# Optimization experiments

Measured on AMD Instinct MI355X. Metric: run time of the kernel, lower is better.

Reference implementation:

```python
import jax, jax.numpy as jnp
import numpy as np

DIM, HEADS, WS, SHIFT = 192, 6, 8, 4
EPS = 1e-5


def layer_norm(x, g, b):
    mu = jnp.mean(x, axis=-1, keepdims=True)
    var = jnp.mean(jnp.square(x - mu), axis=-1, keepdims=True)
    return (x - mu) * jax.lax.rsqrt(var + EPS) * g + b


def window_partition(x, ws):
    # x: [B, H, W, C] -> [B*nW, ws*ws, C]
    B, H, W, C = x.shape
    x = x.reshape(B, H // ws, ws, W // ws, ws, C)
    return x.transpose(0, 1, 3, 2, 4, 5).reshape(-1, ws * ws, C)


def window_merge(win, ws, B, H, W, C):
    x = win.reshape(B, H // ws, W // ws, ws, ws, C)
    return x.transpose(0, 1, 3, 2, 4, 5).reshape(B, H, W, C)


def make_shift_mask(H, W, ws, shift):
    # standard Swin attention mask for shifted windows (host-side constant)
    img = np.zeros((H, W), dtype=np.float32)
    cnt = 0
    slices = (slice(0, -ws), slice(-ws, -shift), slice(-shift, None))
    for hs in slices:
        for wsl in slices:
            img[hs, wsl] = cnt
            cnt += 1
    m = img.reshape(H // ws, ws, W // ws, ws).transpose(0, 2, 1, 3).reshape(-1, ws * ws)  # [nW, N]
    diff = m[:, None, :] - m[:, :, None]
    return jnp.asarray(np.where(diff != 0, -100.0, 0.0).astype(np.float32))  # [nW, N, N]


def swin_attention(x, qkv_w, qkv_b, proj_w, proj_b, shift):
    B, H, W, C = x.shape
    h, d = HEADS, C // HEADS
    scale = 1.0 / jnp.sqrt(jnp.asarray(d, x.dtype))
    if shift > 0:
        x = jnp.roll(x, shift=(-shift, -shift), axis=(1, 2))
    win = window_partition(x, WS)                       # [Bn, N, C]
    Bn, N, _ = win.shape
    qkv = win @ qkv_w + qkv_b                           # [Bn, N, 3C]
    qkv = qkv.reshape(Bn, N, 3, h, d).transpose(2, 0, 3, 1, 4)
    q, k, v = qkv[0], qkv[1], qkv[2]                    # [Bn, h, N, d]
    attn = jnp.einsum('bhnd,bhmd->bhnm', q, k) * scale  # [Bn, h, N, N]
    if shift > 0:
        mask = make_shift_mask(H, W, WS, shift)         # [nW, N, N]
        nW = mask.shape[0]
        attn = attn.reshape(Bn // nW, nW, h, N, N) + mask[None, :, None]
        attn = attn.reshape(Bn, h, N, N)
    attn = jax.nn.softmax(attn, axis=-1)
    out = jnp.einsum('bhnm,bhmd->bhnd', attn, v)        # [Bn, h, N, d]
    out = out.transpose(0, 2, 1, 3).reshape(Bn, N, C)
    out = out @ proj_w + proj_b
    out = window_merge(out, WS, B, H, W, C)
    if shift > 0:
        out = jnp.roll(out, shift=(shift, shift), axis=(1, 2))
    return out


def setup_inputs() -> dict:
    key = jax.random.key(0)
    ks = jax.random.split(key, 6)
    B, H, W, C = 8, 128, 128, DIM
    s = 0.02
    return {
        'x': jax.random.normal(ks[0], (B, H, W, C), jnp.float32),
        'ln1_g': jnp.ones((C,), jnp.float32),
        'ln1_b': jnp.zeros((C,), jnp.float32),
        'qkv1_w': jax.random.normal(ks[1], (C, 3 * C), jnp.float32) * s,
        'qkv1_b': jnp.zeros((3 * C,), jnp.float32),
        'proj1_w': jax.random.normal(ks[2], (C, C), jnp.float32) * s,
        'proj1_b': jnp.zeros((C,), jnp.float32),
        'ln2_g': jnp.ones((C,), jnp.float32),
        'ln2_b': jnp.zeros((C,), jnp.float32),
        'qkv2_w': jax.random.normal(ks[3], (C, 3 * C), jnp.float32) * s,
        'qkv2_b': jnp.zeros((3 * C,), jnp.float32),
        'proj2_w': jax.random.normal(ks[4], (C, C), jnp.float32) * s,
        'proj2_b': jnp.zeros((C,), jnp.float32),
    }


def reference(x, ln1_g, ln1_b, qkv1_w, qkv1_b, proj1_w, proj1_b,
              ln2_g, ln2_b, qkv2_w, qkv2_b, proj2_w, proj2_b):
    # W-MSA branch (mlp1 is an empty Sequential -> identity)
    y = layer_norm(x, ln1_g, ln1_b)
    x = x + swin_attention(y, qkv1_w, qkv1_b, proj1_w, proj1_b, shift=0)
    # SW-MSA branch (mlp2 is identity)
    y = layer_norm(x, ln2_g, ln2_b)
    x = x + swin_attention(y, qkv2_w, qkv2_b, proj2_w, proj2_b, shift=SHIFT)
    return x
```

## Files before the change

kernel.cpp:

```cpp
#include <hip/hip_runtime.h>

typedef unsigned int   u32;
typedef unsigned short u16;
typedef __bf16 bf16x8 __attribute__((ext_vector_type(8)));
typedef float  f32x4  __attribute__((ext_vector_type(4)));

__device__ __forceinline__ u16 f2bf(float f) {
    u32 u = __builtin_bit_cast(u32, f);
    u += 0x7FFFu + ((u >> 16) & 1u);
    return (u16)(u >> 16);
}
__device__ __forceinline__ u32 pk2bf(float a, float b) {
    return (u32)f2bf(a) | ((u32)f2bf(b) << 16);
}
__device__ __forceinline__ bf16x8 ldfrag(const u16* p) {
    return __builtin_bit_cast(bf16x8, *reinterpret_cast<const uint4*>(p));
}

__device__ __forceinline__ u32 swz(u32 i) { return i ^ ((i >> 3) & 7u); }

template<int SHIFT>
__global__ __launch_bounds__(768) void swin_branch(
    const float* __restrict__ xin, float* __restrict__ xout,
    const float* __restrict__ ln_g, const float* __restrict__ ln_b,
    const u16*   __restrict__ wqkv_t,
    const float* __restrict__ qkv_b,
    const u16*   __restrict__ wproj_t,
    const float* __restrict__ proj_b)
{
    __shared__ __align__(16) u16 smem[49152];
    __shared__ float red1[2][6][64];
    __shared__ float red2[2][6][64];
    constexpr u32 QOFF = 12288;

    const int tid  = threadIdx.x;
    const int win  = (tid >= 384) ? 1 : 0;
    const int lt   = tid - win*384;
    const int wid  = lt >> 6;
    const int lane = lt & 63;
    const int lr   = lane & 15;
    const int lg   = lane >> 4;
    const u32 lsw  = swz((u32)lane);
    const u32 SB   = (u32)win * 24576u;

    const int Wid = blockIdx.x*2 + win;
    const int b   = Wid >> 8;
    const int wy  = (Wid >> 4) & 15;
    const int wx  = Wid & 15;

    {
        const int ty = lane >> 3, tx = lane & 7;
        const int shy = (wy*8 + ty + SHIFT) & 127;
        const int shx = (wx*8 + tx + SHIFT) & 127;
        const float* xp = xin + ((size_t)((b*128 + shy)*128 + shx))*192 + wid*32;
        float xv[32];
        float s1 = 0.f, s2 = 0.f;
        #pragma unroll
        for (int j = 0; j < 8; ++j) {
            float4 v = reinterpret_cast<const float4*>(xp)[j];
            xv[j*4+0]=v.x; xv[j*4+1]=v.y; xv[j*4+2]=v.z; xv[j*4+3]=v.w;
            s1 += v.x+v.y+v.z+v.w;
            s2 += v.x*v.x + v.y*v.y + v.z*v.z + v.w*v.w;
        }
        red1[win][wid][lane] = s1; red2[win][wid][lane] = s2;
        __syncthreads();
        float a1 = 0.f, a2 = 0.f;
        #pragma unroll
        for (int w = 0; w < 6; ++w) { a1 += red1[win][w][lane]; a2 += red2[win][w][lane]; }
        const float mu = a1 * (1.f/192.f);
        const float rs = rsqrtf(a2 * (1.f/192.f) - mu*mu + 1e-5f);
        const float* gp = ln_g + wid*32;
        const float* bp = ln_b + wid*32;
        const u32 yblk = SB + (u32)((lg*6 + wid)*512);
        #pragma unroll
        for (int cc8 = 0; cc8 < 4; ++cc8) {
            u32 pk[4];
            #pragma unroll
            for (int q = 0; q < 4; ++q) {
                int j = cc8*8 + q*2;
                float y0 = (xv[j]   - mu)*rs*gp[j]   + bp[j];
                float y1 = (xv[j+1] - mu)*rs*gp[j+1] + bp[j+1];
                pk[q] = pk2bf(y0, y1);
            }
            *reinterpret_cast<uint4*>(&smem[yblk + swz((u32)(lr + 16*cc8))*8]) =
                make_uint4(pk[0],pk[1],pk[2],pk[3]);
        }
    }
    __syncthreads();

    uint2 kpk[4][2];
    uint2 vpk[4][2];
    {
        {
            f32x4 acc[4][4];
            #pragma unroll
            for (int mi=0; mi<4; ++mi)
                #pragma unroll
                for (int t=0; t<4; ++t) acc[mi][t] = f32x4{0.f,0.f,0.f,0.f};
            #pragma unroll
            for (int ks=0; ks<6; ++ks) {
                bf16x8 af[4];
                #pragma unroll
                for (int mi=0; mi<4; ++mi)
                    af[mi] = ldfrag(&smem[SB + (u32)((mi*6+ks)*512) + lsw*8]);
                bf16x8 bw[4];
                #pragma unroll
                for (int t=0; t<4; ++t)
                    bw[t] = ldfrag(&wqkv_t[((t>>1)*192 + wid*32 + (t&1)*16 + lr)*192 + 32*ks + 8*lg]);
                #pragma unroll
                for (int mi=0; mi<4; ++mi)
                    #pragma unroll
                    for (int t=0; t<4; ++t)
                        acc[mi][t] = __builtin_amdgcn_mfma_f32_16x16x32_bf16(af[mi], bw[t], acc[mi][t], 0,0,0);
            }
            #pragma unroll
            for (int t=0; t<2; ++t) {
                const float bias = qkv_b[wid*32 + t*16 + lr];
                const u32 lphi   = (u32)(16*(2*t + (lr>>3)));
                #pragma unroll
                for (int mi=0; mi<4; ++mi)
                    #pragma unroll
                    for (int rg=0; rg<4; ++rg) {
                        const u32 pos = (u32)(4*lg + rg) + lphi;
                        smem[SB + QOFF + (u32)(wid*2048) + mi*512 + swz(pos)*8 + (lr&7)] =
                            f2bf((acc[mi][t][rg] + bias) * 0.1767766952966369f);
                    }
            }
            #pragma unroll
            for (int t2=0; t2<2; ++t2) {
                const float bias = qkv_b[192 + wid*32 + t2*16 + lr];
                #pragma unroll
                for (int mi=0; mi<4; ++mi)
                    kpk[mi][t2] = make_uint2(
                        pk2bf(acc[mi][2+t2][0] + bias, acc[mi][2+t2][1] + bias),
                        pk2bf(acc[mi][2+t2][2] + bias, acc[mi][2+t2][3] + bias));
            }
        }
        {
            f32x4 acc[4][2];
            #pragma unroll
            for (int mi=0; mi<4; ++mi)
                #pragma unroll
                for (int t=0; t<2; ++t) acc[mi][t] = f32x4{0.f,0.f,0.f,0.f};
            #pragma unroll
            for (int ks=0; ks<6; ++ks) {
                bf16x8 af[4];
                #pragma unroll
                for (int mi=0; mi<4; ++mi)
                    af[mi] = ldfrag(&smem[SB + (u32)((mi*6+ks)*512) + lsw*8]);
                bf16x8 bw[2];
                #pragma unroll
                for (int t=0; t<2; ++t)
                    bw[t] = ldfrag(&wqkv_t[(384 + wid*32 + t*16 + lr)*192 + 32*ks + 8*lg]);
                #pragma unroll
                for (int mi=0; mi<4; ++mi)
                    #pragma unroll
                    for (int t=0; t<2; ++t)
                        acc[mi][t] = __builtin_amdgcn_mfma_f32_16x16x32_bf16(af[mi], bw[t], acc[mi][t], 0,0,0);
            }
            #pragma unroll
            for (int tv=0; tv<2; ++tv) {
                const float bias = qkv_b[384 + wid*32 + tv*16 + lr];
                #pragma unroll
                for (int mi=0; mi<4; ++mi)
                    vpk[mi][tv] = make_uint2(
                        pk2bf(acc[mi][tv][0] + bias, acc[mi][tv][1] + bias),
                        pk2bf(acc[mi][tv][2] + bias, acc[mi][tv][3] + bias));
            }
        }
    }
    __syncthreads();

    float rsum[4][4];
    f32x4 o_[4][2];
    {
        const u32 W  = SB + (u32)(wid*512);
        const u32 qb = SB + QOFF + (u32)(wid*2048);
        #define BLK(s) ((u32)(s)*3072u + W)

        #pragma unroll
        for (int t2=0; t2<2; ++t2) {
            const u32 lphi = (u32)(16*(2*t2 + (lr>>3)));
            #pragma unroll
            for (int mi=0; mi<4; ++mi) {
                const u32 a0 = BLK(mi) + (lr&7);
                smem[a0 + swz((u32)(4*lg+0) + lphi)*8] = (u16)(kpk[mi][t2].x);
                smem[a0 + swz((u32)(4*lg+1) + lphi)*8] = (u16)(kpk[mi][t2].x >> 16);
                smem[a0 + swz((u32)(4*lg+2) + lphi)*8] = (u16)(kpk[mi][t2].y);
                smem[a0 + swz((u32)(4*lg+3) + lphi)*8] = (u16)(kpk[mi][t2].y >> 16);
            }
        }
        bf16x8 aq[4], bk[4];
        #pragma unroll
        for (int mi=0; mi<4; ++mi) aq[mi] = ldfrag(&smem[qb + mi*512 + lsw*8]);
        #pragma unroll
        for (int ni=0; ni<4; ++ni) bk[ni] = ldfrag(&smem[BLK(ni) + lsw*8]);
        __builtin_amdgcn_sched_barrier(0);

        #pragma unroll
        for (int tv=0; tv<2; ++tv)
            #pragma unroll
            for (int mi=0; mi<4; ++mi) {
                const u32 pos = (u32)(lr + 16*(2*(mi&1) + (lg>>1)));
                *reinterpret_cast<uint2*>(
                    &smem[BLK(tv*2 + (mi>>1)) + swz(pos)*8 + 4*(lg&1)]) = vpk[mi][tv];
            }

        int kl[4];
        if constexpr (SHIFT > 0) {
            #pragma unroll
            for (int ni=0; ni<4; ++ni) {
                const int col = 16*ni + lr;
                const int hu = wy*8 + (col>>3);
                const int wu = wx*8 + (col&7);
                kl[ni] = ((hu >= 124) ? 2 : (hu >= 120 ? 1 : 0))*3
                       + ((wu >= 124) ? 2 : (wu >= 120 ? 1 : 0));
            }
        }
        u32 p16[4][4][2];
        #pragma unroll
        for (int mi=0; mi<4; ++mi) {
            f32x4 sr[4];
            #pragma unroll
            for (int ni=0; ni<4; ++ni)
                sr[ni] = __builtin_amdgcn_mfma_f32_16x16x32_bf16(aq[mi], bk[ni],
                             f32x4{0.f,0.f,0.f,0.f}, 0,0,0);
            #pragma unroll
            for (int rg=0; rg<4; ++rg) {
                int rl = 0;
                if constexpr (SHIFT > 0) {
                    const int row = 16*mi + 4*lg + rg;
                    const int hu = wy*8 + (row>>3);
                    const int wu = wx*8 + (row&7);
                    rl = ((hu >= 124) ? 2 : (hu >= 120 ? 1 : 0))*3
                       + ((wu >= 124) ? 2 : (wu >= 120 ? 1 : 0));
                }
                #pragma unroll
                for (int ni=0; ni<4; ++ni) {
                    float e = __expf(sr[ni][rg]);
                    if constexpr (SHIFT > 0)
                        e = (rl == kl[ni]) ? e : 0.f;
                    sr[ni][rg] = e;
                }
            }
            #pragma unroll
            for (int ni=0; ni<4; ++ni) {
                p16[mi][ni][0] = pk2bf(sr[ni][0], sr[ni][1]);
                p16[mi][ni][1] = pk2bf(sr[ni][2], sr[ni][3]);
            }
        }

        bf16x8 ap0[4], ap1[4];
        #pragma unroll
        for (int mi=0; mi<4; ++mi)
            #pragma unroll
            for (int ni=0; ni<2; ++ni)
                #pragma unroll
                for (int rg=0; rg<4; ++rg) {
                    const u32 pos = (u32)(4*lg + rg + 16*(2*ni + (lr>>3)));
                    smem[qb + mi*512 + swz(pos)*8 + (lr&7)] =
                        (u16)(p16[mi][ni][rg>>1] >> (16*(rg&1)));
                }
        #pragma unroll
        for (int mi=0; mi<4; ++mi) ap0[mi] = ldfrag(&smem[qb + mi*512 + lsw*8]);
        __builtin_amdgcn_sched_barrier(0);
        #pragma unroll
        for (int mi=0; mi<4; ++mi)
            #pragma unroll
            for (int ni=2; ni<4; ++ni)
                #pragma unroll
                for (int rg=0; rg<4; ++rg) {
                    const u32 pos = (u32)(4*lg + rg + 16*(2*(ni-2) + (lr>>3)));
                    smem[qb + mi*512 + swz(pos)*8 + (lr&7)] =
                        (u16)(p16[mi][ni][rg>>1] >> (16*(rg&1)));
                }
        #pragma unroll
        for (int mi=0; mi<4; ++mi) ap1[mi] = ldfrag(&smem[qb + mi*512 + lsw*8]);
        __builtin_amdgcn_sched_barrier(0);

        bf16x8 vones;
        #pragma unroll
        for (int j=0; j<8; ++j) vones[j] = (__bf16)1.0f;
        #pragma unroll
        for (int mi=0; mi<4; ++mi) {
            f32x4 racc = __builtin_amdgcn_mfma_f32_16x16x32_bf16(ap0[mi], vones,
                             f32x4{0.f,0.f,0.f,0.f}, 0,0,0);
            racc = __builtin_amdgcn_mfma_f32_16x16x32_bf16(ap1[mi], vones, racc, 0,0,0);
            #pragma unroll
            for (int rg=0; rg<4; ++rg)
                rsum[mi][rg] = __builtin_amdgcn_rcpf(racc[rg]);
        }

        bf16x8 bv[2][2];
        #pragma unroll
        for (int tv=0; tv<2; ++tv)
            #pragma unroll
            for (int ksv=0; ksv<2; ++ksv)
                bv[tv][ksv] = ldfrag(&smem[BLK(tv*2+ksv) + lsw*8]);

        #pragma unroll
        for (int mi=0; mi<4; ++mi)
            #pragma unroll
            for (int tv=0; tv<2; ++tv) {
                o_[mi][tv] = __builtin_amdgcn_mfma_f32_16x16x32_bf16(ap0[mi], bv[tv][0],
                                 f32x4{0.f,0.f,0.f,0.f}, 0,0,0);
                o_[mi][tv] = __builtin_amdgcn_mfma_f32_16x16x32_bf16(ap1[mi], bv[tv][1],
                                 o_[mi][tv], 0,0,0);
            }
        __builtin_amdgcn_sched_barrier(0);

        #pragma unroll
        for (int mi=0; mi<4; ++mi)
            #pragma unroll
            for (int tv=0; tv<2; ++tv)
                #pragma unroll
                for (int rg=0; rg<4; ++rg) {
                    const u32 pos = (u32)(4*lg + rg + 16*(2*tv + (lr>>3)));
                    smem[BLK(mi) + swz(pos)*8 + (lr&7)] = f2bf(o_[mi][tv][rg] * rsum[mi][rg]);
                }
        #undef BLK
    }
    __syncthreads();

    {
        f32x4 a2[4][2];
        #pragma unroll
        for (int mi=0; mi<4; ++mi)
            #pragma unroll
            for (int ni=0; ni<2; ++ni) a2[mi][ni] = f32x4{0.f,0.f,0.f,0.f};
        #pragma unroll
        for (int ks=0; ks<6; ++ks) {
            bf16x8 af[4], bw[2];
            #pragma unroll
            for (int mi=0; mi<4; ++mi)
                af[mi] = ldfrag(&smem[SB + (u32)((mi*6+ks)*512) + lsw*8]);
            #pragma unroll
            for (int ni=0; ni<2; ++ni)
                bw[ni] = ldfrag(&wproj_t[(wid*32 + 16*ni + lr)*192 + 32*ks + 8*lg]);
            #pragma unroll
            for (int mi=0; mi<4; ++mi)
                #pragma unroll
                for (int ni=0; ni<2; ++ni)
                    a2[mi][ni] = __builtin_amdgcn_mfma_f32_16x16x32_bf16(af[mi], bw[ni], a2[mi][ni], 0,0,0);
        }
        #pragma unroll
        for (int ni=0; ni<2; ++ni) {
            const int c  = wid*32 + 16*ni + lr;
            const float pb = proj_b[c];
            #pragma unroll
            for (int mi=0; mi<4; ++mi)
                #pragma unroll
                for (int rg=0; rg<4; ++rg) {
                    const int row = 16*mi + 4*lg + rg;
                    const int ty = row >> 3, tx = row & 7;
                    const int shy = (wy*8 + ty + SHIFT) & 127;
                    const int shx = (wx*8 + tx + SHIFT) & 127;
                    const size_t idx = ((size_t)((b*128 + shy)*128 + shx))*192 + c;
                    xout[idx] = xin[idx] + a2[mi][ni][rg] + pb;
                }
        }
    }
}

__global__ void prep_weights(const float* __restrict__ qkv1, const float* __restrict__ proj1,
                             const float* __restrict__ qkv2, const float* __restrict__ proj2,
                             u16* __restrict__ ws)
{
    const int i = blockIdx.x*blockDim.x + threadIdx.x;
    if (i < 110592) {
        const int n = i / 192, k = i - n*192;
        ws[i]          = f2bf(qkv1[k*576 + n]);
        ws[147456 + i] = f2bf(qkv2[k*576 + n]);
    }
    if (i < 36864) {
        const int n = i / 192, k = i - n*192;
        ws[110592 + i] = f2bf(proj1[k*192 + n]);
        ws[258048 + i] = f2bf(proj2[k*192 + n]);
    }
}

extern "C" void kernel_launch(void* const* d_in, const int* in_sizes, int n_in,
                              void* d_out, int out_size, void* d_ws, size_t ws_size,
                              hipStream_t stream)
{
    const float* x       = (const float*)d_in[0];
    const float* ln1_g   = (const float*)d_in[1];
    const float* ln1_b   = (const float*)d_in[2];
    const float* qkv1_w  = (const float*)d_in[3];
    const float* qkv1_b  = (const float*)d_in[4];
    const float* proj1_w = (const float*)d_in[5];
    const float* proj1_b = (const float*)d_in[6];
    const float* ln2_g   = (const float*)d_in[7];
    const float* ln2_b   = (const float*)d_in[8];
    const float* qkv2_w  = (const float*)d_in[9];
    const float* qkv2_b  = (const float*)d_in[10];
    const float* proj2_w = (const float*)d_in[11];
    const float* proj2_b = (const float*)d_in[12];
    float* out = (float*)d_out;
    u16*   wsp = (u16*)d_ws;

    prep_weights<<<dim3(432), dim3(256), 0, stream>>>(qkv1_w, proj1_w, qkv2_w, proj2_w, wsp);
    swin_branch<0><<<dim3(1024), dim3(768), 0, stream>>>(x,   out, ln1_g, ln1_b,
                                                         wsp,        qkv1_b, wsp+110592, proj1_b);
    swin_branch<4><<<dim3(1024), dim3(768), 0, stream>>>(out, out, ln2_g, ln2_b,
                                                         wsp+147456, qkv2_b, wsp+258048, proj2_b);
}
```

Baseline: 268.0 us.

## Transpose attention MFMA operands for packed LDS stores and hardware bf16 conversion

Swaps MFMA operand order so the QKV, score and PV accumulators come out transposed. Each lane can then write four contiguous bf16 values with one 64-bit LDS store instead of four scalar 16-bit stores. The software bf16 rounding is replaced by the v_cvt_pk_bf16_f32 instruction, and log2(e) is folded into the Q scale so exp2f can replace __expf. Row sums are now computed with a ones-matrix as the A operand, and V is staged in the Q buffer. This reworks the fragment layout across all attention stages, which risks subtle indexing or mask-orientation errors.

```diff
diff --git a/kernel.cpp b/kernel.cpp
--- a/kernel.cpp
+++ b/kernel.cpp
@@ -10,8 +10,10 @@
     u += 0x7FFFu + ((u >> 16) & 1u);
     return (u16)(u >> 16);
 }
-__device__ __forceinline__ u32 pk2bf(float a, float b) {
-    return (u32)f2bf(a) | ((u32)f2bf(b) << 16);
+__device__ __forceinline__ u32 cvtpk(float a, float b) {
+    u32 r;
+    asm("v_cvt_pk_bf16_f32 %0, %1, %2" : "=v"(r) : "v"(a), "v"(b));
+    return r;
 }
 __device__ __forceinline__ bf16x8 ldfrag(const u16* p) {
     return __builtin_bit_cast(bf16x8, *reinterpret_cast<const uint4*>(p));
@@ -32,6 +34,7 @@
     __shared__ float red1[2][6][64];
     __shared__ float red2[2][6][64];
     constexpr u32 QOFF = 12288;
+    constexpr float QSC = 0.17677669529663689f * 1.4426950408889634f;
 
     const int tid  = threadIdx.x;
     const int win  = (tid >= 384) ? 1 : 0;
@@ -80,7 +83,7 @@
                 int j = cc8*8 + q*2;
                 float y0 = (xv[j]   - mu)*rs*gp[j]   + bp[j];
                 float y1 = (xv[j+1] - mu)*rs*gp[j+1] + bp[j+1];
-                pk[q] = pk2bf(y0, y1);
+                pk[q] = cvtpk(y0, y1);
             }
             *reinterpret_cast<uint4*>(&smem[yblk + swz((u32)(lr + 16*cc8))*8]) =
                 make_uint4(pk[0],pk[1],pk[2],pk[3]);
@@ -111,29 +114,31 @@
                 for (int mi=0; mi<4; ++mi)
                     #pragma unroll
                     for (int t=0; t<4; ++t)
-                        acc[mi][t] = __builtin_amdgcn_mfma_f32_16x16x32_bf16(af[mi], bw[t], acc[mi][t], 0,0,0);
+                        acc[mi][t] = __builtin_amdgcn_mfma_f32_16x16x32_bf16(bw[t], af[mi], acc[mi][t], 0,0,0);
             }
             #pragma unroll
             for (int t=0; t<2; ++t) {
-                const float bias = qkv_b[wid*32 + t*16 + lr];
-                const u32 lphi   = (u32)(16*(2*t + (lr>>3)));
-                #pragma unroll
-                for (int mi=0; mi<4; ++mi)
-                    #pragma unroll
-                    for (int rg=0; rg<4; ++rg) {
-                        const u32 pos = (u32)(4*lg + rg) + lphi;
-                        smem[SB + QOFF + (u32)(wid*2048) + mi*512 + swz(pos)*8 + (lr&7)] =
-                            f2bf((acc[mi][t][rg] + bias) * 0.1767766952966369f);
-                    }
+                const float4 b4 = *reinterpret_cast<const float4*>(&qkv_b[wid*32 + t*16 + 4*lg]);
+                const u32 chunk = (u32)lr + 16u*(u32)(2*t + (lg>>1));
+                #pragma unroll
+                for (int mi=0; mi<4; ++mi) {
+                    float v0 = (acc[mi][t][0] + b4.x) * QSC;
+                    float v1 = (acc[mi][t][1] + b4.y) * QSC;
+                    float v2 = (acc[mi][t][2] + b4.z) * QSC;
+                    float v3 = (acc[mi][t][3] + b4.w) * QSC;
+                    *reinterpret_cast<uint2*>(
+                        &smem[SB + QOFF + (u32)(wid*2048) + mi*512 + swz(chunk)*8 + 4*(lg&1)]) =
+                        make_uint2(cvtpk(v0,v1), cvtpk(v2,v3));
+                }
             }
             #pragma unroll
             for (int t2=0; t2<2; ++t2) {
-                const float bias = qkv_b[192 + wid*32 + t2*16 + lr];
+                const float4 b4 = *reinterpret_cast<const float4*>(&qkv_b[192 + wid*32 + t2*16 + 4*lg]);
                 #pragma unroll
                 for (int mi=0; mi<4; ++mi)
                     kpk[mi][t2] = make_uint2(
-                        pk2bf(acc[mi][2+t2][0] + bias, acc[mi][2+t2][1] + bias),
-                        pk2bf(acc[mi][2+t2][2] + bias, acc[mi][2+t2][3] + bias));
+                        cvtpk(acc[mi][2+t2][0] + b4.x, acc[mi][2+t2][1] + b4.y),
+                        cvtpk(acc[mi][2+t2][2] + b4.z, acc[mi][2+t2][3] + b4.w));
             }
         }
         {
@@ -164,160 +169,147 @@
                 #pragma unroll
                 for (int mi=0; mi<4; ++mi)
                     vpk[mi][tv] = make_uint2(
-                        pk2bf(acc[mi][tv][0] + bias, acc[mi][tv][1] + bias),
-                        pk2bf(acc[mi][tv][2] + bias, acc[mi][tv][3] + bias));
+                        cvtpk(acc[mi][tv][0] + bias, acc[mi][tv][1] + bias),
+                        cvtpk(acc[mi][tv][2] + bias, acc[mi][tv][3] + bias));
             }
         }
     }
     __syncthreads();
 
-    float rsum[4][4];
-    f32x4 o_[4][2];
+    float rsum[4];
+    f32x4 o_[2][4];
     {
         const u32 W  = SB + (u32)(wid*512);
-        const u32 qb = SB + QOFF + (u32)(wid*2048);
+        const u32 QB = SB + QOFF + (u32)(wid*2048);
         #define BLK(s) ((u32)(s)*3072u + W)
 
         #pragma unroll
         for (int t2=0; t2<2; ++t2) {
-            const u32 lphi = (u32)(16*(2*t2 + (lr>>3)));
-            #pragma unroll
-            for (int mi=0; mi<4; ++mi) {
-                const u32 a0 = BLK(mi) + (lr&7);
-                smem[a0 + swz((u32)(4*lg+0) + lphi)*8] = (u16)(kpk[mi][t2].x);
-                smem[a0 + swz((u32)(4*lg+1) + lphi)*8] = (u16)(kpk[mi][t2].x >> 16);
-                smem[a0 + swz((u32)(4*lg+2) + lphi)*8] = (u16)(kpk[mi][t2].y);
-                smem[a0 + swz((u32)(4*lg+3) + lphi)*8] = (u16)(kpk[mi][t2].y >> 16);
-            }
-        }
-        bf16x8 aq[4], bk[4];
-        #pragma unroll
-        for (int mi=0; mi<4; ++mi) aq[mi] = ldfrag(&smem[qb + mi*512 + lsw*8]);
-        #pragma unroll
-        for (int ni=0; ni<4; ++ni) bk[ni] = ldfrag(&smem[BLK(ni) + lsw*8]);
+            const u32 chunk = (u32)lr + 16u*(u32)(2*t2 + (lg>>1));
+            #pragma unroll
+            for (int mi=0; mi<4; ++mi)
+                *reinterpret_cast<uint2*>(
+                    &smem[BLK(mi) + swz(chunk)*8 + 4*(lg&1)]) = kpk[mi][t2];
+        }
+        bf16x8 ak[4], bq[4];
+        #pragma unroll
+        for (int mi=0; mi<4; ++mi) ak[mi] = ldfrag(&smem[BLK(mi) + lsw*8]);
+        #pragma unroll
+        for (int nq=0; nq<4; ++nq) bq[nq] = ldfrag(&smem[QB + nq*512 + lsw*8]);
         __builtin_amdgcn_sched_barrier(0);
 
-        #pragma unroll
-        for (int tv=0; tv<2; ++tv)
-            #pragma unroll
-            for (int mi=0; mi<4; ++mi) {
-                const u32 pos = (u32)(lr + 16*(2*(mi&1) + (lg>>1)));
-                *reinterpret_cast<uint2*>(
-                    &smem[BLK(tv*2 + (mi>>1)) + swz(pos)*8 + 4*(lg&1)]) = vpk[mi][tv];
-            }
-
-        int kl[4];
+        int qcl[4];
         if constexpr (SHIFT > 0) {
             #pragma unroll
-            for (int ni=0; ni<4; ++ni) {
-                const int col = 16*ni + lr;
-                const int hu = wy*8 + (col>>3);
-                const int wu = wx*8 + (col&7);
-                kl[ni] = ((hu >= 124) ? 2 : (hu >= 120 ? 1 : 0))*3
-                       + ((wu >= 124) ? 2 : (wu >= 120 ? 1 : 0));
-            }
-        }
-        u32 p16[4][4][2];
+            for (int nq=0; nq<4; ++nq) {
+                const int qt = 16*nq + lr;
+                const int hu = wy*8 + (qt>>3);
+                const int wu = wx*8 + (qt&7);
+                qcl[nq] = ((hu >= 124) ? 2 : (hu >= 120 ? 1 : 0))*3
+                        + ((wu >= 124) ? 2 : (wu >= 120 ? 1 : 0));
+            }
+        }
+
+        uint2 p16[4][4];
         #pragma unroll
         for (int mi=0; mi<4; ++mi) {
             f32x4 sr[4];
             #pragma unroll
-            for (int ni=0; ni<4; ++ni)
-                sr[ni] = __builtin_amdgcn_mfma_f32_16x16x32_bf16(aq[mi], bk[ni],
+            for (int nq=0; nq<4; ++nq)
+                sr[nq] = __builtin_amdgcn_mfma_f32_16x16x32_bf16(ak[mi], bq[nq],
                              f32x4{0.f,0.f,0.f,0.f}, 0,0,0);
             #pragma unroll
             for (int rg=0; rg<4; ++rg) {
-                int rl = 0;
+                int kcl = 0;
                 if constexpr (SHIFT > 0) {
-                    const int row = 16*mi + 4*lg + rg;
-                    const int hu = wy*8 + (row>>3);
-                    const int wu = wx*8 + (row&7);
-                    rl = ((hu >= 124) ? 2 : (hu >= 120 ? 1 : 0))*3
-                       + ((wu >= 124) ? 2 : (wu >= 120 ? 1 : 0));
+                    const int kt = 16*mi + 4*lg + rg;
+                    const int hu = wy*8 + (kt>>3);
+                    const int wu = wx*8 + (kt&7);
+                    kcl = ((hu >= 124) ? 2 : (hu >= 120 ? 1 : 0))*3
+                        + ((wu >= 124) ? 2 : (wu >= 120 ? 1 : 0));
                 }
                 #pragma unroll
-                for (int ni=0; ni<4; ++ni) {
-                    float e = __expf(sr[ni][rg]);
+                for (int nq=0; nq<4; ++nq) {
+                    float e = exp2f(sr[nq][rg]);
                     if constexpr (SHIFT > 0)
-                        e = (rl == kl[ni]) ? e : 0.f;
-                    sr[ni][rg] = e;
+                        e = (kcl == qcl[nq]) ? e : 0.f;
+                    sr[nq][rg] = e;
                 }
             }
             #pragma unroll
-            for (int ni=0; ni<4; ++ni) {
-                p16[mi][ni][0] = pk2bf(sr[ni][0], sr[ni][1]);
-                p16[mi][ni][1] = pk2bf(sr[ni][2], sr[ni][3]);
-            }
-        }
-
-        bf16x8 ap0[4], ap1[4];
-        #pragma unroll
-        for (int mi=0; mi<4; ++mi)
-            #pragma unroll
-            for (int ni=0; ni<2; ++ni)
-                #pragma unroll
-                for (int rg=0; rg<4; ++rg) {
-                    const u32 pos = (u32)(4*lg + rg + 16*(2*ni + (lr>>3)));
-                    smem[qb + mi*512 + swz(pos)*8 + (lr&7)] =
-                        (u16)(p16[mi][ni][rg>>1] >> (16*(rg&1)));
-                }
-        #pragma unroll
-        for (int mi=0; mi<4; ++mi) ap0[mi] = ldfrag(&smem[qb + mi*512 + lsw*8]);
+            for (int nq=0; nq<4; ++nq)
+                p16[mi][nq] = make_uint2(cvtpk(sr[nq][0], sr[nq][1]),
+                                         cvtpk(sr[nq][2], sr[nq][3]));
+        }
+
+        #pragma unroll
+        for (int mi=0; mi<4; ++mi) {
+            const u32 chunk = (u32)lr + 16u*(u32)(2*(mi&1) + (lg>>1));
+            #pragma unroll
+            for (int nq=0; nq<4; ++nq) {
+                const u32 base = (mi >> 1) ? BLK(nq) : (QB + nq*512);
+                *reinterpret_cast<uint2*>(&smem[base + swz(chunk)*8 + 4*(lg&1)]) = p16[mi][nq];
+            }
+        }
+        bf16x8 bp[4][2];
+        #pragma unroll
+        for (int nq=0; nq<4; ++nq) {
+            bp[nq][0] = ldfrag(&smem[QB + nq*512 + lsw*8]);
+            bp[nq][1] = ldfrag(&smem[BLK(nq) + lsw*8]);
+        }
         __builtin_amdgcn_sched_barrier(0);
-        #pragma unroll
-        for (int mi=0; mi<4; ++mi)
-            #pragma unroll
-            for (int ni=2; ni<4; ++ni)
-                #pragma unroll
-                for (int rg=0; rg<4; ++rg) {
-                    const u32 pos = (u32)(4*lg + rg + 16*(2*(ni-2) + (lr>>3)));
-                    smem[qb + mi*512 + swz(pos)*8 + (lr&7)] =
-                        (u16)(p16[mi][ni][rg>>1] >> (16*(rg&1)));
-                }
-        #pragma unroll
-        for (int mi=0; mi<4; ++mi) ap1[mi] = ldfrag(&smem[qb + mi*512 + lsw*8]);
+
+        bf16x8 aones;
+        {
+            const u32 one2 = 0x3F803F80u;
+            aones = __builtin_bit_cast(bf16x8, make_uint4(one2, one2, one2, one2));
+        }
+        #pragma unroll
+        for (int nq=0; nq<4; ++nq) {
+            f32x4 racc = __builtin_amdgcn_mfma_f32_16x16x32_bf16(aones, bp[nq][0],
+                             f32x4{0.f,0.f,0.f,0.f}, 0,0,0);
+            racc = __builtin_amdgcn_mfma_f32_16x16x32_bf16(aones, bp[nq][1], racc, 0,0,0);
+            rsum[nq] = __builtin_amdgcn_rcpf(racc[0]);
+        }
+
+        #pragma unroll
+        for (int mi=0; mi<4; ++mi) {
+            const u32 chunk = (u32)lr + 16u*(u32)(2*(mi&1) + (lg>>1));
+            #pragma unroll
+            for (int tv=0; tv<2; ++tv)
+                *reinterpret_cast<uint2*>(
+                    &smem[QB + (u32)((2*tv + (mi>>1))*512) + swz(chunk)*8 + 4*(lg&1)]) = vpk[mi][tv];
+        }
+        bf16x8 av[2][2];
+        #pragma unroll
+        for (int dv=0; dv<2; ++dv)
+            #pragma unroll
+            for (int ks=0; ks<2; ++ks)
+                av[dv][ks] = ldfrag(&smem[QB + (u32)((2*dv + ks)*512) + lsw*8]);
         __builtin_amdgcn_sched_barrier(0);
 
-        bf16x8 vones;
-        #pragma unroll
-        for (int j=0; j<8; ++j) vones[j] = (__bf16)1.0f;
-        #pragma unroll
-        for (int mi=0; mi<4; ++mi) {
-            f32x4 racc = __builtin_amdgcn_mfma_f32_16x16x32_bf16(ap0[mi], vones,
-                             f32x4{0.f,0.f,0.f,0.f}, 0,0,0);
-            racc = __builtin_amdgcn_mfma_f32_16x16x32_bf16(ap1[mi], vones, racc, 0,0,0);
-            #pragma unroll
-            for (int rg=0; rg<4; ++rg)
-                rsum[mi][rg] = __builtin_amdgcn_rcpf(racc[rg]);
-        }
-
-        bf16x8 bv[2][2];
-        #pragma unroll
-        for (int tv=0; tv<2; ++tv)
-            #pragma unroll
-            for (int ksv=0; ksv<2; ++ksv)
-                bv[tv][ksv] = ldfrag(&smem[BLK(tv*2+ksv) + lsw*8]);
-
-        #pragma unroll
-        for (int mi=0; mi<4; ++mi)
-            #pragma unroll
-            for (int tv=0; tv<2; ++tv) {
-                o_[mi][tv] = __builtin_amdgcn_mfma_f32_16x16x32_bf16(ap0[mi], bv[tv][0],
+        #pragma unroll
+        for (int dv=0; dv<2; ++dv)
+            #pragma unroll
+            for (int nq=0; nq<4; ++nq) {
+                o_[dv][nq] = __builtin_amdgcn_mfma_f32_16x16x32_bf16(av[dv][0], bp[nq][0],
                                  f32x4{0.f,0.f,0.f,0.f}, 0,0,0);
-                o_[mi][tv] = __builtin_amdgcn_mfma_f32_16x16x32_bf16(ap1[mi], bv[tv][1],
-                                 o_[mi][tv], 0,0,0);
+                o_[dv][nq] = __builtin_amdgcn_mfma_f32_16x16x32_bf16(av[dv][1], bp[nq][1],
+                                 o_[dv][nq], 0,0,0);
             }
         __builtin_amdgcn_sched_barrier(0);
 
         #pragma unroll
-        for (int mi=0; mi<4; ++mi)
-            #pragma unroll
-            for (int tv=0; tv<2; ++tv)
-                #pragma unroll
-                for (int rg=0; rg<4; ++rg) {
-                    const u32 pos = (u32)(4*lg + rg + 16*(2*tv + (lr>>3)));
-                    smem[BLK(mi) + swz(pos)*8 + (lr&7)] = f2bf(o_[mi][tv][rg] * rsum[mi][rg]);
-                }
+        for (int dv=0; dv<2; ++dv) {
+            const u32 chunk = (u32)lr + 16u*(u32)(2*dv + (lg>>1));
+            #pragma unroll
+            for (int nq=0; nq<4; ++nq) {
+                const float r = rsum[nq];
+                *reinterpret_cast<uint2*>(&smem[BLK(nq) + swz(chunk)*8 + 4*(lg&1)]) =
+                    make_uint2(cvtpk(o_[dv][nq][0]*r, o_[dv][nq][1]*r),
+                               cvtpk(o_[dv][nq][2]*r, o_[dv][nq][3]*r));
+            }
+        }
         #undef BLK
     }
     __syncthreads();
```

New measurement: 262.8 us. About the same (-1.9%).
